# Optimization experiments

Hardware: AMD Instinct MI355X
Metric: run time of the kernel (lower is better)

## Reference

```python
import jax, jax.numpy as jnp
import numpy as np
from jax import lax

SCORE_THRESHOLD = 0.001
IOU_THRESHOLD = 0.7
MAX_DETECTIONS = 300
PRE_NMS_TOPK = 1024      # standard pre-NMS candidate cap (torchvision/YOLO practice)
CLASS_OFFSET = 4096.0    # > max image coord, separates classes so cross-class IoU == 0
IMG = 640.0

B, N, C = 32, 8400, 80


def setup_inputs() -> dict:
    key = jax.random.key(0)
    kc, ks, kp = jax.random.split(key, 3)
    # well-formed boxes in [y1, x1, y2, x2] convention (matches repo's nms())
    tl = jax.random.uniform(kc, (B, N, 2), jnp.float32, 0.0, IMG - 1.0)   # (y1, x1)
    wh = jax.random.uniform(ks, (B, N, 2), jnp.float32, 4.0, 160.0)      # (h, w)
    boxes = jnp.concatenate([tl, jnp.minimum(tl + wh, IMG)], axis=-1)     # [B,N,4]
    scores = jax.random.uniform(kp, (B, N, C), jnp.float32)               # [B,N,C]
    return {"boxes": boxes, "scores": scores}


def _pairwise_iou(b):
    # b: [B,K,4] as [y1,x1,y2,x2]; +1 pixel convention per the repo's nms()
    y1, x1, y2, x2 = b[..., 0], b[..., 1], b[..., 2], b[..., 3]
    areas = (x2 - x1 + 1.0) * (y2 - y1 + 1.0)                             # [B,K]
    yy1 = jnp.maximum(y1[:, :, None], y1[:, None, :])
    xx1 = jnp.maximum(x1[:, :, None], x1[:, None, :])
    yy2 = jnp.minimum(y2[:, :, None], y2[:, None, :])
    xx2 = jnp.minimum(x2[:, :, None], x2[:, None, :])
    w = jnp.maximum(0.0, xx2 - xx1 + 1.0)
    h = jnp.maximum(0.0, yy2 - yy1 + 1.0)
    inter = w * h                                                          # [B,K,K]
    return inter / (areas[:, :, None] + areas[:, None, :] - inter)


def multiclass_nms(boxes, scores):
    b, n, c = scores.shape
    flat = jnp.where(scores > SCORE_THRESHOLD, scores, 0.0).reshape(b, n * c)
    top_scores, top_idx = lax.top_k(flat, PRE_NMS_TOPK)                    # [B,K]
    box_idx = top_idx // c
    cls_idx = top_idx % c                                                  # int32 [B,K]
    cand = jnp.take_along_axis(boxes, box_idx[..., None], axis=1)          # [B,K,4]
    # offset boxes by class so per-class NMS happens in one shared pass
    off = cand + (cls_idx.astype(cand.dtype) * CLASS_OFFSET)[..., None]
    iou = _pairwise_iou(off)                                               # [B,K,K]

    k = PRE_NMS_TOPK
    idx = jnp.arange(k)
    keep0 = top_scores > SCORE_THRESHOLD                                   # [B,K]

    def body(i, keep):
        row = iou[:, i, :]                                                 # [B,K]
        sup = (row > IOU_THRESHOLD) & keep[:, i][:, None] & (idx[None, :] > i)
        return keep & ~sup

    keep = lax.fori_loop(0, k, body, keep0)                                # greedy NMS

    final_scores = jnp.where(keep, top_scores, 0.0)
    out_scores, sel = lax.top_k(final_scores, MAX_DETECTIONS)              # [B,300]
    out_boxes = jnp.take_along_axis(cand, sel[..., None], axis=1)          # [B,300,4]
    out_labels = jnp.take_along_axis(cls_idx, sel, axis=1)                 # [B,300]
    n_valid = jnp.minimum(jnp.sum(keep, axis=1, keepdims=True), MAX_DETECTIONS)
    return out_boxes, out_scores, out_labels.astype(jnp.int32), n_valid.astype(jnp.int32)


def reference(boxes, scores):
    return multiclass_nms(boxes, scores)
```

## Files before the change

kernel.cpp:

```cpp
#include <hip/hip_runtime.h>
#include <cstdint>
#include <cstddef>

#define B_      32
#define N_      8400
#define C_      80
#define NC      672000
#define NCV4    168000
#define NBINS   4096
#define TOPK    1024
#define MAXDET  300
#define CANDCAP 4096
#define NSLICE  16
#define SLICE_V4 10500
#define NBKT    8
#define SEGB    64
#define BSORT   256

#define STAGE_THRESH 0.998046875f

#define WS_SEGKEYS  0
#define WS_SEGCNT   2097152
#define WS_FBFLAG   2113536
#define WS_TOPSCORE 2113664
#define WS_TOPBOX   2244736
#define WS_TOPCLS   2769024
#define WS_KEEP     2900096

#define OUT_SCORES  38400
#define OUT_LABELS  48000
#define OUT_NVALID  57600

__global__ __launch_bounds__(256) void stage_kernel(const float4* __restrict__ scores4,
                                                    unsigned* __restrict__ segCnt,
                                                    unsigned long long* __restrict__ segKeys) {
    __shared__ unsigned lcnt[NBKT];
    int b = blockIdx.x, sl = blockIdx.y, tid = threadIdx.x;
    if (tid < NBKT) lcnt[tid] = 0;
    __syncthreads();
    const float4* s = scores4 + (size_t)b * NCV4 + (size_t)sl * SLICE_V4;
    for (int i = tid; i < SLICE_V4; i += 256) {
        float4 v = s[i];
        float c[4] = {v.x, v.y, v.z, v.w};
        unsigned flat0 = ((unsigned)sl * SLICE_V4 + (unsigned)i) * 4u;
        #pragma unroll
        for (int kc = 0; kc < 4; ++kc) {
            float x = (c[kc] > 0.001f) ? c[kc] : 0.0f;
            if (x >= STAGE_THRESH) {
                int bin = (int)(x * 4096.0f);
                bin = bin > (NBINS - 1) ? (NBINS - 1) : bin;
                int bkt = bin - 4088;
                unsigned p = atomicAdd(&lcnt[bkt], 1u);
                if (p < (unsigned)SEGB)
                    segKeys[(((size_t)(b * NBKT + bkt)) * NSLICE + sl) * SEGB + p] =
                        ((unsigned long long)__float_as_uint(x) << 32) |
                        (unsigned long long)(0xFFFFFFFFu - (flat0 + kc));
            }
        }
    }
    __syncthreads();
    if (tid < NBKT) segCnt[(b * NBKT + tid) * NSLICE + sl] = lcnt[tid];
}

__global__ __launch_bounds__(64) void sortb_kernel(
        const unsigned long long* __restrict__ segKeys,
        const unsigned* __restrict__ segCnt,
        const float4* __restrict__ boxes4,
        unsigned* __restrict__ fbFlag,
        float* __restrict__ topScore,
        float4* __restrict__ topBox4,
        int* __restrict__ topCls) {
    __shared__ unsigned long long k[BSORT];
    __shared__ unsigned bsum[NBKT];
    __shared__ unsigned bok[NBKT];
    __shared__ unsigned spref[NSLICE + 1];
    int b = blockIdx.x, bkt = blockIdx.y, lane = threadIdx.x;

    if (lane < NBKT) {
        const unsigned* c = segCnt + (b * NBKT + lane) * NSLICE;
        unsigned ssum = 0, ok = 1;
        for (int sl = 0; sl < NSLICE; ++sl) {
            unsigned v = c[sl];
            if (v > (unsigned)SEGB) ok = 0;
            ssum += v;
        }
        bsum[lane] = ssum; bok[lane] = ok;
    }
    __threadfence_block();
    unsigned M = 0, base = 0; int valid = 1;
    #pragma unroll
    for (int t = 0; t < NBKT; ++t) {
        unsigned s2 = bsum[t];
        if (!bok[t] || s2 > (unsigned)BSORT) valid = 0;
        M += s2;
        if (t > bkt) base += s2;
    }
    unsigned n = bsum[bkt];
    if (M < (unsigned)TOPK || M > (unsigned)CANDCAP) valid = 0;
    if (bkt == 0 && lane == 0) fbFlag[b] = valid ? 0u : 1u;
    if (!valid || base >= (unsigned)TOPK || n == 0) return;

    if (lane == 0) {
        unsigned acc = 0; spref[0] = 0;
        const unsigned* c = segCnt + (b * NBKT + bkt) * NSLICE;
        for (int sl = 0; sl < NSLICE; ++sl) { acc += c[sl]; spref[sl + 1] = acc; }
    }
    __threadfence_block();
    for (int sl = 0; sl < NSLICE; ++sl) {
        unsigned b0 = spref[sl], c2 = spref[sl + 1] - b0;
        const unsigned long long* src =
            segKeys + (((size_t)(b * NBKT + bkt)) * NSLICE + sl) * SEGB;
        for (unsigned t = lane; t < c2; t += 64) k[b0 + t] = src[t];
    }
    for (unsigned t = n + lane; t < (unsigned)BSORT; t += 64) k[t] = 0ull;
    __threadfence_block();

    for (int kk = 2; kk <= BSORT; kk <<= 1) {
        for (int j = kk >> 1; j > 0; j >>= 1) {
            for (int c2 = lane; c2 < BSORT / 2; c2 += 64) {
                int t = ((c2 & ~(j - 1)) << 1) | (c2 & (j - 1));
                int l = t | j;
                unsigned long long a0 = k[t], c0 = k[l];
                bool sw = ((t & kk) == 0) ? (a0 < c0) : (a0 > c0);
                if (sw) { k[t] = c0; k[l] = a0; }
            }
            __threadfence_block();
        }
    }

    unsigned wlim = (unsigned)TOPK - base; if (wlim > n) wlim = n;
    for (unsigned r = lane; r < wlim; r += 64) {
        unsigned long long key = k[r];
        float sc = __uint_as_float((unsigned)(key >> 32));
        unsigned idx = 0xFFFFFFFFu - (unsigned)(key & 0xFFFFFFFFull);
        if (idx >= (unsigned)NC) idx = 0;
        unsigned bi = idx / (unsigned)C_;
        unsigned cl = idx - bi * (unsigned)C_;
        unsigned pos = base + r;
        topScore[b * TOPK + pos] = sc;
        topBox4[b * TOPK + pos] = boxes4[(size_t)b * N_ + bi];
        topCls[b * TOPK + pos] = (int)cl;
    }
}

__global__ __launch_bounds__(1024) void fallback_kernel(
        const float4* __restrict__ scores4,
        const unsigned* __restrict__ fbFlag,
        const float* __restrict__ boxes,
        float* __restrict__ topScore,
        float* __restrict__ topBox,
        int* __restrict__ topCls) {
    int b = blockIdx.x;
    if (fbFlag[b] == 0) return;
    __shared__ union {
        unsigned long long k[CANDCAP];
        unsigned fh[NBINS];
    } u;
    __shared__ unsigned scnt;
    __shared__ int s_cut;
    int tid = threadIdx.x;
    for (int i2 = tid; i2 < NBINS; i2 += 1024) u.fh[i2] = 0;
    if (tid == 0) scnt = 0;
    __syncthreads();
    const float4* s = scores4 + (size_t)b * NCV4;
    for (int i2 = tid; i2 < NCV4; i2 += 1024) {
        float4 v = s[i2];
        float c4[4] = {v.x, v.y, v.z, v.w};
        #pragma unroll
        for (int kc = 0; kc < 4; ++kc) {
            float x = (c4[kc] > 0.001f) ? c4[kc] : 0.0f;
            int bin = (int)(x * 4096.0f);
            bin = bin > (NBINS - 1) ? (NBINS - 1) : bin;
            atomicAdd(&u.fh[bin], 1u);
        }
    }
    __syncthreads();
    if (tid == 0) {
        unsigned acc = 0; int cb = 0;
        for (int bin = NBINS - 1; bin >= 0; --bin) {
            acc += u.fh[bin];
            if (acc >= (unsigned)TOPK) { cb = bin; break; }
        }
        s_cut = cb;
    }
    __syncthreads();
    int cb = s_cut;
    for (int i2 = tid; i2 < NCV4; i2 += 1024) {
        float4 v = s[i2];
        float c4[4] = {v.x, v.y, v.z, v.w};
        unsigned flat0 = (unsigned)i2 * 4u;
        #pragma unroll
        for (int kc = 0; kc < 4; ++kc) {
            float x = (c4[kc] > 0.001f) ? c4[kc] : 0.0f;
            int bin = (int)(x * 4096.0f);
            bin = bin > (NBINS - 1) ? (NBINS - 1) : bin;
            if (bin >= cb) {
                unsigned p = atomicAdd(&scnt, 1u);
                if (p < (unsigned)CANDCAP)
                    u.k[p] = ((unsigned long long)__float_as_uint(x) << 32) |
                             (unsigned long long)(0xFFFFFFFFu - (flat0 + kc));
            }
        }
    }
    __syncthreads();
    unsigned M = scnt; if (M > (unsigned)CANDCAP) M = CANDCAP;
    int S = (M <= 1024u) ? 1024 : (M <= 2048u ? 2048 : CANDCAP);
    for (int i2 = tid; i2 < S; i2 += 1024)
        if (i2 >= (int)M) u.k[i2] = 0ull;
    __syncthreads();
    for (int kk = 2; kk <= S; kk <<= 1) {
        for (int j = kk >> 1; j > 0; j >>= 1) {
            for (int t = tid; t < S; t += 1024) {
                int l = t ^ j;
                if (l > t) {
                    unsigned long long a0 = u.k[t], c0 = u.k[l];
                    bool sw = ((t & kk) == 0) ? (a0 < c0) : (a0 > c0);
                    if (sw) { u.k[t] = c0; u.k[l] = a0; }
                }
            }
            __syncthreads();
        }
    }
    unsigned long long key = u.k[tid];
    float sc = __uint_as_float((unsigned)(key >> 32));
    unsigned idx = 0xFFFFFFFFu - (unsigned)(key & 0xFFFFFFFFull);
    if (idx >= (unsigned)NC) idx = 0;
    unsigned bi = idx / (unsigned)C_;
    unsigned cl = idx - bi * (unsigned)C_;
    const float* bp = boxes + (size_t)b * N_ * 4 + (size_t)bi * 4;
    float c0 = bp[0], c1 = bp[1], c2 = bp[2], c3 = bp[3];
    topScore[b * TOPK + tid] = sc;
    float* tb = topBox + ((size_t)b * TOPK + tid) * 4;
    tb[0] = c0; tb[1] = c1; tb[2] = c2; tb[3] = c3;
    topCls[b * TOPK + tid] = (int)cl;
}

#define CLS_CAP 256
__global__ __launch_bounds__(64) void nms_kernel(const float* __restrict__ topScore,
                                                 const float* __restrict__ topBox,
                                                 const int* __restrict__ topCls,
                                                 int* __restrict__ keep) {
    __shared__ unsigned short pos[CLS_CAP];
    __shared__ float by1[CLS_CAP], bx1[CLS_CAP], by2[CLS_CAP], bx2[CLS_CAP];
    __shared__ float barea[CLS_CAP];
    __shared__ unsigned char sup[CLS_CAP];
    int b = blockIdx.x;
    int c = blockIdx.y;
    int lane = threadIdx.x;
    const float* ts = topScore + b * TOPK;
    const int*   tc = topCls + b * TOPK;
    int*         kp = keep + b * TOPK;
    float off = (float)c * 4096.0f;
    int base = 0;
    for (int chunkS = 0; chunkS < TOPK; chunkS += 64) {
        int i = chunkS + lane;
        int cls = tc[i];
        float sc = ts[i];
        bool mine = (cls == c);
        bool listed = mine && (sc > 0.001f);
        if (mine) kp[i] = 0;
        unsigned long long mask = __ballot(listed);
        int rank = __popcll(mask & ((1ull << lane) - 1ull));
        if (listed) {
            int slot = base + rank;
            if (slot < CLS_CAP) {
                pos[slot] = (unsigned short)i;
                const float* tb = topBox + ((size_t)(b * TOPK + i)) * 4;
                float y1 = tb[0] + off, x1 = tb[1] + off;
                float y2 = tb[2] + off, x2 = tb[3] + off;
                by1[slot] = y1; bx1[slot] = x1; by2[slot] = y2; bx2[slot] = x2;
                barea[slot] = __fmul_rn((x2 - x1) + 1.0f, (y2 - y1) + 1.0f);
                sup[slot] = 0;
            }
        }
        base += __popcll(mask);
    }
    int m = base < CLS_CAP ? base : CLS_CAP;
    __syncthreads();
    int cur = 0;
    while (cur < m) {
        if (lane == 0) kp[pos[cur]] = 1;
        float cy1 = by1[cur], cx1 = bx1[cur], cy2 = by2[cur], cx2 = bx2[cur];
        float carea = barea[cur];
        for (int j = cur + 1 + lane; j < m; j += 64) {
            if (!sup[j]) {
                float yy1 = fmaxf(cy1, by1[j]), xx1 = fmaxf(cx1, bx1[j]);
                float yy2 = fminf(cy2, by2[j]), xx2 = fminf(cx2, bx2[j]);
                float w = fmaxf(0.0f, (xx2 - xx1) + 1.0f);
                float h = fmaxf(0.0f, (yy2 - yy1) + 1.0f);
                float inter = __fmul_rn(w, h);
                float denom = (carea + barea[j]) - inter;
                float iou = inter / denom;
                if (iou > 0.7f) sup[j] = 1;
            }
        }
        __syncthreads();
        int nxt = m;
        for (int j = cur + 1 + lane; j < m; j += 64)
            if (!sup[j]) { nxt = j; break; }
        for (int o = 32; o > 0; o >>= 1) {
            int other = __shfl_xor(nxt, o, 64);
            nxt = nxt < other ? nxt : other;
        }
        cur = nxt;
    }
}

__global__ __launch_bounds__(1024) void finalize_kernel(const float* __restrict__ topScore,
                                                        const float* __restrict__ topBox,
                                                        const int* __restrict__ topCls,
                                                        const int* __restrict__ keep,
                                                        float* __restrict__ out) {
    __shared__ int sk[TOPK];
    __shared__ int sel[MAXDET];
    int b = blockIdx.x;
    int i = threadIdx.x;
    int kp = keep[b * TOPK + i];
    sk[i] = kp;
    __syncthreads();
    for (int off = 1; off < TOPK; off <<= 1) {
        int add = (i >= off) ? sk[i - off] : 0;
        __syncthreads();
        sk[i] += add;
        __syncthreads();
    }
    int nk = sk[TOPK - 1];
    int incl = sk[i];
    int kexcl = incl - kp;
    int sexcl = i - kexcl;
    if (kp) {
        if (kexcl < MAXDET) sel[kexcl] = i;
    } else {
        int slot = nk + sexcl;
        if (slot < MAXDET) sel[slot] = i;
    }
    __syncthreads();
    if (i < MAXDET) {
        int p = sel[i];
        float sc = (i < nk) ? topScore[b * TOPK + p] : 0.0f;
        const float* tb = topBox + ((size_t)b * TOPK + p) * 4;
        float* ob = out + ((size_t)b * MAXDET + i) * 4;
        ob[0] = tb[0]; ob[1] = tb[1]; ob[2] = tb[2]; ob[3] = tb[3];
        out[OUT_SCORES + b * MAXDET + i] = sc;
        out[OUT_LABELS + b * MAXDET + i] = (float)topCls[b * TOPK + p];
    }
    if (i == 0) out[OUT_NVALID + b] = (float)(nk < MAXDET ? nk : MAXDET);
}

extern "C" void kernel_launch(void* const* d_in, const int* in_sizes, int n_in,
                              void* d_out, int out_size, void* d_ws, size_t ws_size,
                              hipStream_t stream) {
    const float* boxes  = (const float*)d_in[0];
    const float* scores = (const float*)d_in[1];
    float* out = (float*)d_out;
    char* ws = (char*)d_ws;

    unsigned long long* segKeys = (unsigned long long*)(ws + WS_SEGKEYS);
    unsigned* segCnt = (unsigned*)(ws + WS_SEGCNT);
    unsigned* fbFlag = (unsigned*)(ws + WS_FBFLAG);
    float* topScore = (float*)(ws + WS_TOPSCORE);
    float* topBox = (float*)(ws + WS_TOPBOX);
    int* topCls = (int*)(ws + WS_TOPCLS);
    int* keep = (int*)(ws + WS_KEEP);

    const float4* scores4 = (const float4*)scores;
    const float4* boxes4  = (const float4*)boxes;

    stage_kernel<<<dim3(B_, NSLICE), 256, 0, stream>>>(scores4, segCnt, segKeys);
    sortb_kernel<<<dim3(B_, NBKT), 64, 0, stream>>>(segKeys, segCnt, boxes4, fbFlag,
                                                    topScore, (float4*)topBox, topCls);
    fallback_kernel<<<B_, 1024, 0, stream>>>(scores4, fbFlag, boxes,
                                             topScore, topBox, topCls);
    nms_kernel<<<dim3(B_, C_), 64, 0, stream>>>(topScore, topBox, topCls, keep);
    finalize_kernel<<<B_, 1024, 0, stream>>>(topScore, topBox, topCls, keep, out);
}
```

Baseline: 190.5 us.

## Fold fallback into sort kernel and fuse finalize into NMS via last-block counter

Merges the fallback top-k path into the bucket-sort kernel, where only one 64-lane block per batch runs it when the staged candidates are invalid. The finalize step is moved into the NMS kernel: each class block atomically bumps a per-batch counter, and the last block does a wave-level prefix scan and writes the outputs. This removes two kernel launches and the 1024-thread fallback/finalize blocks. The fallback now runs on a single wave, so it is much slower whenever it triggers, and correctness relies on threadfence and counter ordering.

```diff
diff --git a/kernel.cpp b/kernel.cpp
--- a/kernel.cpp
+++ b/kernel.cpp
@@ -16,16 +16,17 @@
 #define NBKT    8
 #define SEGB    64
 #define BSORT   256
+#define CTRS    32
 
 #define STAGE_THRESH 0.998046875f
 
 #define WS_SEGKEYS  0
 #define WS_SEGCNT   2097152
-#define WS_FBFLAG   2113536
-#define WS_TOPSCORE 2113664
-#define WS_TOPBOX   2244736
-#define WS_TOPCLS   2769024
-#define WS_KEEP     2900096
+#define WS_NMSCTR   2113536
+#define WS_TOPSCORE 2117632
+#define WS_TOPBOX   2248704
+#define WS_TOPCLS   2772992
+#define WS_KEEP     2904064
 
 #define OUT_SCORES  38400
 #define OUT_LABELS  48000
@@ -33,10 +34,12 @@
 
 __global__ __launch_bounds__(256) void stage_kernel(const float4* __restrict__ scores4,
                                                     unsigned* __restrict__ segCnt,
-                                                    unsigned long long* __restrict__ segKeys) {
+                                                    unsigned long long* __restrict__ segKeys,
+                                                    unsigned* __restrict__ nmsCtr) {
     __shared__ unsigned lcnt[NBKT];
     int b = blockIdx.x, sl = blockIdx.y, tid = threadIdx.x;
     if (tid < NBKT) lcnt[tid] = 0;
+    if (sl == 0 && tid == 0) nmsCtr[b * CTRS] = 0;
     __syncthreads();
     const float4* s = scores4 + (size_t)b * NCV4 + (size_t)sl * SLICE_V4;
     for (int i = tid; i < SLICE_V4; i += 256) {
@@ -63,17 +66,19 @@
 }
 
 __global__ __launch_bounds__(64) void sortb_kernel(
+        const float4* __restrict__ scores4,
         const unsigned long long* __restrict__ segKeys,
         const unsigned* __restrict__ segCnt,
         const float4* __restrict__ boxes4,
-        unsigned* __restrict__ fbFlag,
         float* __restrict__ topScore,
         float4* __restrict__ topBox4,
         int* __restrict__ topCls) {
-    __shared__ unsigned long long k[BSORT];
+    __shared__ unsigned long long kbuf[CANDCAP];
     __shared__ unsigned bsum[NBKT];
     __shared__ unsigned bok[NBKT];
     __shared__ unsigned spref[NSLICE + 1];
+    __shared__ unsigned scnt;
+    __shared__ int s_cut;
     int b = blockIdx.x, bkt = blockIdx.y, lane = threadIdx.x;
 
     if (lane < NBKT) {
@@ -97,73 +102,58 @@
     }
     unsigned n = bsum[bkt];
     if (M < (unsigned)TOPK || M > (unsigned)CANDCAP) valid = 0;
-    if (bkt == 0 && lane == 0) fbFlag[b] = valid ? 0u : 1u;
-    if (!valid || base >= (unsigned)TOPK || n == 0) return;
-
-    if (lane == 0) {
-        unsigned acc = 0; spref[0] = 0;
-        const unsigned* c = segCnt + (b * NBKT + bkt) * NSLICE;
-        for (int sl = 0; sl < NSLICE; ++sl) { acc += c[sl]; spref[sl + 1] = acc; }
-    }
-    __threadfence_block();
-    for (int sl = 0; sl < NSLICE; ++sl) {
-        unsigned b0 = spref[sl], c2 = spref[sl + 1] - b0;
-        const unsigned long long* src =
-            segKeys + (((size_t)(b * NBKT + bkt)) * NSLICE + sl) * SEGB;
-        for (unsigned t = lane; t < c2; t += 64) k[b0 + t] = src[t];
-    }
-    for (unsigned t = n + lane; t < (unsigned)BSORT; t += 64) k[t] = 0ull;
-    __threadfence_block();
-
-    for (int kk = 2; kk <= BSORT; kk <<= 1) {
-        for (int j = kk >> 1; j > 0; j >>= 1) {
-            for (int c2 = lane; c2 < BSORT / 2; c2 += 64) {
-                int t = ((c2 & ~(j - 1)) << 1) | (c2 & (j - 1));
-                int l = t | j;
-                unsigned long long a0 = k[t], c0 = k[l];
-                bool sw = ((t & kk) == 0) ? (a0 < c0) : (a0 > c0);
-                if (sw) { k[t] = c0; k[l] = a0; }
-            }
-            __threadfence_block();
-        }
-    }
-
-    unsigned wlim = (unsigned)TOPK - base; if (wlim > n) wlim = n;
-    for (unsigned r = lane; r < wlim; r += 64) {
-        unsigned long long key = k[r];
-        float sc = __uint_as_float((unsigned)(key >> 32));
-        unsigned idx = 0xFFFFFFFFu - (unsigned)(key & 0xFFFFFFFFull);
-        if (idx >= (unsigned)NC) idx = 0;
-        unsigned bi = idx / (unsigned)C_;
-        unsigned cl = idx - bi * (unsigned)C_;
-        unsigned pos = base + r;
-        topScore[b * TOPK + pos] = sc;
-        topBox4[b * TOPK + pos] = boxes4[(size_t)b * N_ + bi];
-        topCls[b * TOPK + pos] = (int)cl;
-    }
-}
-
-__global__ __launch_bounds__(1024) void fallback_kernel(
-        const float4* __restrict__ scores4,
-        const unsigned* __restrict__ fbFlag,
-        const float* __restrict__ boxes,
-        float* __restrict__ topScore,
-        float* __restrict__ topBox,
-        int* __restrict__ topCls) {
-    int b = blockIdx.x;
-    if (fbFlag[b] == 0) return;
-    __shared__ union {
-        unsigned long long k[CANDCAP];
-        unsigned fh[NBINS];
-    } u;
-    __shared__ unsigned scnt;
-    __shared__ int s_cut;
-    int tid = threadIdx.x;
-    for (int i2 = tid; i2 < NBINS; i2 += 1024) u.fh[i2] = 0;
-    if (tid == 0) scnt = 0;
-    __syncthreads();
+
+    if (valid) {
+        if (base >= (unsigned)TOPK || n == 0) return;
+        if (lane == 0) {
+            unsigned acc = 0; spref[0] = 0;
+            const unsigned* c = segCnt + (b * NBKT + bkt) * NSLICE;
+            for (int sl = 0; sl < NSLICE; ++sl) { acc += c[sl]; spref[sl + 1] = acc; }
+        }
+        __threadfence_block();
+        for (int sl = 0; sl < NSLICE; ++sl) {
+            unsigned b0 = spref[sl], c2 = spref[sl + 1] - b0;
+            const unsigned long long* src =
+                segKeys + (((size_t)(b * NBKT + bkt)) * NSLICE + sl) * SEGB;
+            for (unsigned t = lane; t < c2; t += 64) kbuf[b0 + t] = src[t];
+        }
+        for (unsigned t = n + lane; t < (unsigned)BSORT; t += 64) kbuf[t] = 0ull;
+        __threadfence_block();
+        for (int kk = 2; kk <= BSORT; kk <<= 1) {
+            for (int j = kk >> 1; j > 0; j >>= 1) {
+                for (int c2 = lane; c2 < BSORT / 2; c2 += 64) {
+                    int t = ((c2 & ~(j - 1)) << 1) | (c2 & (j - 1));
+                    int l = t | j;
+                    unsigned long long a0 = kbuf[t], c0 = kbuf[l];
+                    bool sw = ((t & kk) == 0) ? (a0 < c0) : (a0 > c0);
+                    if (sw) { kbuf[t] = c0; kbuf[l] = a0; }
+                }
+                __threadfence_block();
+            }
+        }
+        unsigned wlim = (unsigned)TOPK - base; if (wlim > n) wlim = n;
+        for (unsigned r = lane; r < wlim; r += 64) {
+            unsigned long long key = kbuf[r];
+            float sc = __uint_as_float((unsigned)(key >> 32));
+            unsigned idx = 0xFFFFFFFFu - (unsigned)(key & 0xFFFFFFFFull);
+            if (idx >= (unsigned)NC) idx = 0;
+            unsigned bi = idx / (unsigned)C_;
+            unsigned cl = idx - bi * (unsigned)C_;
+            unsigned pos = base + r;
+            topScore[b * TOPK + pos] = sc;
+            topBox4[b * TOPK + pos] = boxes4[(size_t)b * N_ + bi];
+            topCls[b * TOPK + pos] = (int)cl;
+        }
+        return;
+    }
+
+    if (bkt != 0) return;
+    unsigned* fh = (unsigned*)kbuf;
+    for (int i2 = lane; i2 < NBINS; i2 += 64) fh[i2] = 0;
+    if (lane == 0) scnt = 0;
+    __threadfence_block();
     const float4* s = scores4 + (size_t)b * NCV4;
-    for (int i2 = tid; i2 < NCV4; i2 += 1024) {
+    for (int i2 = lane; i2 < NCV4; i2 += 64) {
         float4 v = s[i2];
         float c4[4] = {v.x, v.y, v.z, v.w};
         #pragma unroll
@@ -171,21 +161,21 @@
             float x = (c4[kc] > 0.001f) ? c4[kc] : 0.0f;
             int bin = (int)(x * 4096.0f);
             bin = bin > (NBINS - 1) ? (NBINS - 1) : bin;
-            atomicAdd(&u.fh[bin], 1u);
-        }
-    }
-    __syncthreads();
-    if (tid == 0) {
+            atomicAdd(&fh[bin], 1u);
+        }
+    }
+    __threadfence_block();
+    if (lane == 0) {
         unsigned acc = 0; int cb = 0;
         for (int bin = NBINS - 1; bin >= 0; --bin) {
-            acc += u.fh[bin];
+            acc += fh[bin];
             if (acc >= (unsigned)TOPK) { cb = bin; break; }
         }
         s_cut = cb;
     }
-    __syncthreads();
+    __threadfence_block();
     int cb = s_cut;
-    for (int i2 = tid; i2 < NCV4; i2 += 1024) {
+    for (int i2 = lane; i2 < NCV4; i2 += 64) {
         float4 v = s[i2];
         float c4[4] = {v.x, v.y, v.z, v.w};
         unsigned flat0 = (unsigned)i2 * 4u;
@@ -197,53 +187,55 @@
             if (bin >= cb) {
                 unsigned p = atomicAdd(&scnt, 1u);
                 if (p < (unsigned)CANDCAP)
-                    u.k[p] = ((unsigned long long)__float_as_uint(x) << 32) |
-                             (unsigned long long)(0xFFFFFFFFu - (flat0 + kc));
-            }
-        }
-    }
-    __syncthreads();
-    unsigned M = scnt; if (M > (unsigned)CANDCAP) M = CANDCAP;
-    int S = (M <= 1024u) ? 1024 : (M <= 2048u ? 2048 : CANDCAP);
-    for (int i2 = tid; i2 < S; i2 += 1024)
-        if (i2 >= (int)M) u.k[i2] = 0ull;
-    __syncthreads();
+                    kbuf[p] = ((unsigned long long)__float_as_uint(x) << 32) |
+                              (unsigned long long)(0xFFFFFFFFu - (flat0 + kc));
+            }
+        }
+    }
+    __threadfence_block();
+    unsigned M2 = scnt; if (M2 > (unsigned)CANDCAP) M2 = CANDCAP;
+    int S = (M2 <= 1024u) ? 1024 : (M2 <= 2048u ? 2048 : CANDCAP);
+    for (int i2 = (int)M2 + lane; i2 < S; i2 += 64) kbuf[i2] = 0ull;
+    __threadfence_block();
     for (int kk = 2; kk <= S; kk <<= 1) {
         for (int j = kk >> 1; j > 0; j >>= 1) {
-            for (int t = tid; t < S; t += 1024) {
+            for (int t = lane; t < S; t += 64) {
                 int l = t ^ j;
                 if (l > t) {
-                    unsigned long long a0 = u.k[t], c0 = u.k[l];
+                    unsigned long long a0 = kbuf[t], c0 = kbuf[l];
                     bool sw = ((t & kk) == 0) ? (a0 < c0) : (a0 > c0);
-                    if (sw) { u.k[t] = c0; u.k[l] = a0; }
+                    if (sw) { kbuf[t] = c0; kbuf[l] = a0; }
                 }
             }
-            __syncthreads();
-        }
-    }
-    unsigned long long key = u.k[tid];
-    float sc = __uint_as_float((unsigned)(key >> 32));
-    unsigned idx = 0xFFFFFFFFu - (unsigned)(key & 0xFFFFFFFFull);
-    if (idx >= (unsigned)NC) idx = 0;
-    unsigned bi = idx / (unsigned)C_;
-    unsigned cl = idx - bi * (unsigned)C_;
-    const float* bp = boxes + (size_t)b * N_ * 4 + (size_t)bi * 4;
-    float c0 = bp[0], c1 = bp[1], c2 = bp[2], c3 = bp[3];
-    topScore[b * TOPK + tid] = sc;
-    float* tb = topBox + ((size_t)b * TOPK + tid) * 4;
-    tb[0] = c0; tb[1] = c1; tb[2] = c2; tb[3] = c3;
-    topCls[b * TOPK + tid] = (int)cl;
+            __threadfence_block();
+        }
+    }
+    for (int r = lane; r < TOPK; r += 64) {
+        unsigned long long key = kbuf[r];
+        float sc = __uint_as_float((unsigned)(key >> 32));
+        unsigned idx = 0xFFFFFFFFu - (unsigned)(key & 0xFFFFFFFFull);
+        if (idx >= (unsigned)NC) idx = 0;
+        unsigned bi = idx / (unsigned)C_;
+        unsigned cl = idx - bi * (unsigned)C_;
+        topScore[b * TOPK + r] = sc;
+        topBox4[b * TOPK + r] = boxes4[(size_t)b * N_ + bi];
+        topCls[b * TOPK + r] = (int)cl;
+    }
 }
 
 #define CLS_CAP 256
-__global__ __launch_bounds__(64) void nms_kernel(const float* __restrict__ topScore,
-                                                 const float* __restrict__ topBox,
-                                                 const int* __restrict__ topCls,
-                                                 int* __restrict__ keep) {
+__global__ __launch_bounds__(64) void nms_fin_kernel(const float* __restrict__ topScore,
+                                                     const float* __restrict__ topBox,
+                                                     const int* __restrict__ topCls,
+                                                     int* __restrict__ keep,
+                                                     unsigned* __restrict__ nmsCtr,
+                                                     float* __restrict__ out) {
     __shared__ unsigned short pos[CLS_CAP];
     __shared__ float by1[CLS_CAP], bx1[CLS_CAP], by2[CLS_CAP], bx2[CLS_CAP];
     __shared__ float barea[CLS_CAP];
     __shared__ unsigned char sup[CLS_CAP];
+    __shared__ int sel[MAXDET];
+    __shared__ unsigned s_done;
     int b = blockIdx.x;
     int c = blockIdx.y;
     int lane = threadIdx.x;
@@ -304,47 +296,50 @@
         }
         cur = nxt;
     }
-}
-
-__global__ __launch_bounds__(1024) void finalize_kernel(const float* __restrict__ topScore,
-                                                        const float* __restrict__ topBox,
-                                                        const int* __restrict__ topCls,
-                                                        const int* __restrict__ keep,
-                                                        float* __restrict__ out) {
-    __shared__ int sk[TOPK];
-    __shared__ int sel[MAXDET];
-    int b = blockIdx.x;
-    int i = threadIdx.x;
-    int kp = keep[b * TOPK + i];
-    sk[i] = kp;
+
+    __threadfence();
+    if (lane == 0) s_done = atomicAdd(&nmsCtr[b * CTRS], 1u);
     __syncthreads();
-    for (int off = 1; off < TOPK; off <<= 1) {
-        int add = (i >= off) ? sk[i - off] : 0;
-        __syncthreads();
-        sk[i] += add;
-        __syncthreads();
-    }
-    int nk = sk[TOPK - 1];
-    int incl = sk[i];
-    int kexcl = incl - kp;
-    int sexcl = i - kexcl;
-    if (kp) {
-        if (kexcl < MAXDET) sel[kexcl] = i;
-    } else {
-        int slot = nk + sexcl;
-        if (slot < MAXDET) sel[slot] = i;
-    }
-    __syncthreads();
-    if (i < MAXDET) {
-        int p = sel[i];
-        float sc = (i < nk) ? topScore[b * TOPK + p] : 0.0f;
-        const float* tb = topBox + ((size_t)b * TOPK + p) * 4;
-        float* ob = out + ((size_t)b * MAXDET + i) * 4;
-        ob[0] = tb[0]; ob[1] = tb[1]; ob[2] = tb[2]; ob[3] = tb[3];
-        out[OUT_SCORES + b * MAXDET + i] = sc;
-        out[OUT_LABELS + b * MAXDET + i] = (float)topCls[b * TOPK + p];
-    }
-    if (i == 0) out[OUT_NVALID + b] = (float)(nk < MAXDET ? nk : MAXDET);
+    if (s_done != (unsigned)(C_ - 1)) return;
+    __threadfence();
+
+    int lb = lane * 16;
+    int kv[16];
+    int loc[16];
+    int csum = 0;
+    #pragma unroll
+    for (int t = 0; t < 16; ++t) {
+        kv[t] = kp[lb + t];
+        loc[t] = csum;
+        csum += kv[t];
+    }
+    int incl = csum;
+    for (int o = 1; o < 64; o <<= 1) {
+        int y = __shfl_up(incl, o, 64);
+        if (lane >= o) incl += y;
+    }
+    int nk = __shfl(incl, 63, 64);
+    int cexcl = incl - csum;
+    #pragma unroll
+    for (int t = 0; t < 16; ++t) {
+        int i = lb + t;
+        int kexcl = cexcl + loc[t];
+        if (kv[t]) {
+            if (kexcl < MAXDET) sel[kexcl] = i;
+        } else {
+            int slot = nk + (i - kexcl);
+            if (slot < MAXDET) sel[slot] = i;
+        }
+    }
+    __threadfence_block();
+    for (int r = lane; r < MAXDET; r += 64) {
+        int p = sel[r];
+        float sc = (r < nk) ? ts[p] : 0.0f;
+        ((float4*)out)[b * MAXDET + r] = ((const float4*)topBox)[b * TOPK + p];
+        out[OUT_SCORES + b * MAXDET + r] = sc;
+        out[OUT_LABELS + b * MAXDET + r] = (float)tc[p];
+    }
+    if (lane == 0) out[OUT_NVALID + b] = (float)(nk < MAXDET ? nk : MAXDET);
 }
 
 extern "C" void kernel_launch(void* const* d_in, const int* in_sizes, int n_in,
@@ -357,7 +352,7 @@
 
     unsigned long long* segKeys = (unsigned long long*)(ws + WS_SEGKEYS);
     unsigned* segCnt = (unsigned*)(ws + WS_SEGCNT);
-    unsigned* fbFlag = (unsigned*)(ws + WS_FBFLAG);
+    unsigned* nmsCtr = (unsigned*)(ws + WS_NMSCTR);
     float* topScore = (float*)(ws + WS_TOPSCORE);
     float* topBox = (float*)(ws + WS_TOPBOX);
     int* topCls = (int*)(ws + WS_TOPCLS);
@@ -366,11 +361,9 @@
     const float4* scores4 = (const float4*)scores;
     const float4* boxes4  = (const float4*)boxes;
 
-    stage_kernel<<<dim3(B_, NSLICE), 256, 0, stream>>>(scores4, segCnt, segKeys);
-    sortb_kernel<<<dim3(B_, NBKT), 64, 0, stream>>>(segKeys, segCnt, boxes4, fbFlag,
+    stage_kernel<<<dim3(B_, NSLICE), 256, 0, stream>>>(scores4, segCnt, segKeys, nmsCtr);
+    sortb_kernel<<<dim3(B_, NBKT), 64, 0, stream>>>(scores4, segKeys, segCnt, boxes4,
                                                     topScore, (float4*)topBox, topCls);
-    fallback_kernel<<<B_, 1024, 0, stream>>>(scores4, fbFlag, boxes,
-                                             topScore, topBox, topCls);
-    nms_kernel<<<dim3(B_, C_), 64, 0, stream>>>(topScore, topBox, topCls, keep);
-    finalize_kernel<<<B_, 1024, 0, stream>>>(topScore, topBox, topCls, keep, out);
+    nms_fin_kernel<<<dim3(B_, C_), 64, 0, stream>>>(topScore, topBox, topCls, keep,
+                                                    nmsCtr, out);
 }
```

After: 233.6 us. +22.6%, slower.
